# Kernel optimization log

Hardware: AMD Instinct MI355X
Metric: run time of the kernel (lower is better)

Reference implementation:

```python
import jax, jax.numpy as jnp
import numpy as np

N = 4096      # nodes in the propagation tree batch
D = 5000      # input (BoW/TF-IDF) feature dim
H = 512       # hidden_dim
C = 4         # n_class
L = 8         # number of tree levels


def setup_inputs() -> dict:
    key = jax.random.key(0)
    ks = jax.random.split(key, 12)
    init = lambda k, shape, fan: (jax.random.normal(k, shape, jnp.float32)
                                  / np.float32(np.sqrt(fan)))
    x = jax.random.normal(ks[0], (N, D), jnp.float32)
    adj = jax.random.uniform(ks[1], (N, N), jnp.float32)
    level = jax.random.randint(ks[2], (N,), 0, L, jnp.int32)
    return {
        "x": x,
        "adj": adj,
        "level": level,
        "E_w": init(ks[3], (H, D), D),
        "Wr": init(ks[4], (H, H), H),
        "Wz": init(ks[5], (H, H), H),
        "Ur": init(ks[6], (H, H), H),
        "Uz": init(ks[7], (H, H), H),
        "Wh": init(ks[8], (H, H), H),
        "Uh": init(ks[9], (H, H), H),
        "dec_w": init(ks[10], (C, H), H),
        "dec_b": jnp.zeros((C,), jnp.float32),
        "n_levels": L,
    }


def reference(x, adj, level, E_w, Wr, Wz, Ur, Uz, Wh, Uh, dec_w, dec_b, n_levels):
    # x_hat = E(x): [N, H]
    x_hat = x @ E_w.T
    # precompute gate input contributions from x_hat (constant across levels)
    xr = x_hat @ Wr.T
    xz = x_hat @ Wz.T
    xh = x_hat @ Wh.T
    h = jnp.zeros_like(x_hat)  # [N, H]
    # bottom-up over tree levels (deepest level first, root = level 0)
    for j in reversed(range(n_levels)):
        mask = (level == j).astype(x_hat.dtype)[:, None]  # [N, 1]
        # level_adj.mm(h): aggregate children states into current-level rows
        hs = mask * (adj @ h)                              # [N, H]
        r = jax.nn.sigmoid(xr + hs @ Ur.T)
        z = jax.nn.sigmoid(xz + hs @ Uz.T)
        hj_hat = jnp.tanh(xh + (hs * r) @ Uh.T)
        hj = (1.0 - z) * hs + z * hj_hat
        h = h + mask * hj
    # decoder(h): [N, C]
    return h @ dec_w.T + dec_b
```

## Files before the change

### kernel.cpp

```cpp
#include <hip/hip_runtime.h>
#include <math.h>


#define NNODE 4096
#define DD 5000
#define DP 5024
#define HH 512
#define HHHH 262144
#define LL 8
#define PMAX 640
#define AKS 8
#define AKC 512
#define STR 40
#define NHt 2097152
#define XCH 1696
#define EWP (HH * DP)

typedef __attribute__((ext_vector_type(8))) short short8v;
typedef __attribute__((ext_vector_type(4))) float float4v;

union fu { float f; unsigned u; };

__device__ __forceinline__ float sigf(float x) { return 1.0f / (1.0f + __expf(-x)); }
__device__ __forceinline__ float bf2f(ushort b) { fu v; v.u = ((unsigned)b) << 16; return v.f; }

__device__ __forceinline__ void splitpair(float a, float b, unsigned& hi,
                                          unsigned& mi, unsigned& lo) {
  const unsigned M = 0xFFFF0000u;
  fu A, B; A.f = a; B.f = b;
  hi = (A.u >> 16) | (B.u & M);
  fu Ah, Bh; Ah.u = A.u & M; Bh.u = B.u & M;
  float ra = a - Ah.f, rb = b - Bh.f;
  fu A1, B1; A1.f = ra; B1.f = rb;
  mi = (A1.u >> 16) | (B1.u & M);
  fu A1h, B1h; A1h.u = A1.u & M; B1h.u = B1.u & M;
  float ra2 = ra - A1h.f, rb2 = rb - B1h.f;
  fu A2, B2; A2.f = ra2; B2.f = rb2;
  lo = (A2.u >> 16) | (B2.u & M);
}

__device__ __forceinline__ void split8(const float* v, uint4& h, uint4& m, uint4& l) {
  splitpair(v[0], v[1], h.x, m.x, l.x);
  splitpair(v[2], v[3], h.y, m.y, l.y);
  splitpair(v[4], v[5], h.z, m.z, l.z);
  splitpair(v[6], v[7], h.w, m.w, l.w);
}

__device__ __forceinline__ void split1(float x, ushort& h, ushort& m, ushort& l) {
  const unsigned M = 0xFFFF0000u;
  fu a; a.f = x; h = (ushort)(a.u >> 16);
  fu ah; ah.u = a.u & M; float r = x - ah.f;
  fu b; b.f = r; m = (ushort)(b.u >> 16);
  fu bh; bh.u = b.u & M; float r2 = r - bh.f;
  fu c; c.f = r2; l = (ushort)(c.u >> 16);
}

template <int NB, int AROWS, int BROWS>
__device__ __forceinline__ void mfma6(const ushort* As, const ushort* Bs,
                                      int wm, int wn, int lr, int lg8,
                                      float4v (*acc)[NB]) {
  short8v a[2][3];
#pragma unroll
  for (int im = 0; im < 2; ++im)
#pragma unroll
    for (int p = 0; p < 3; ++p)
      a[im][p] = *reinterpret_cast<const short8v*>(
          &As[(p * AROWS + wm + 16 * im + lr) * STR + lg8]);
  short8v b[NB][3];
#pragma unroll
  for (int in = 0; in < NB; ++in)
#pragma unroll
    for (int p = 0; p < 3; ++p)
      b[in][p] = *reinterpret_cast<const short8v*>(
          &Bs[(p * BROWS + wn + 16 * in + lr) * STR + lg8]);
#pragma unroll
  for (int im = 0; im < 2; ++im)
#pragma unroll
    for (int in = 0; in < NB; ++in) {
      float4v c = acc[im][in];
      c = __builtin_amdgcn_mfma_f32_16x16x32_bf16(a[im][0], b[in][0], c, 0, 0, 0);
      c = __builtin_amdgcn_mfma_f32_16x16x32_bf16(a[im][0], b[in][1], c, 0, 0, 0);
      c = __builtin_amdgcn_mfma_f32_16x16x32_bf16(a[im][1], b[in][0], c, 0, 0, 0);
      c = __builtin_amdgcn_mfma_f32_16x16x32_bf16(a[im][0], b[in][2], c, 0, 0, 0);
      c = __builtin_amdgcn_mfma_f32_16x16x32_bf16(a[im][2], b[in][0], c, 0, 0, 0);
      c = __builtin_amdgcn_mfma_f32_16x16x32_bf16(a[im][1], b[in][1], c, 0, 0, 0);
      acc[im][in] = c;
    }
}

__global__ __launch_bounds__(256) void build_lists(const int* __restrict__ level,
                                                   int* __restrict__ counts,
                                                   int* __restrict__ rows, int N) {
  int i = blockIdx.x * blockDim.x + threadIdx.x;
  if (i < N) {
    int j = level[i];
    int p = atomicAdd(&counts[j], 1);
    rows[(size_t)j * N + p] = i;
  }
}

__global__ __launch_bounds__(256) void cast_all(
    const float* __restrict__ Ur, const float* __restrict__ Uz,
    const float* __restrict__ Uh, const float* __restrict__ Wr,
    const float* __restrict__ Wz, const float* __restrict__ Wh,
    ushort* __restrict__ urz3, ushort* __restrict__ uh3,
    ushort* __restrict__ w3s) {
  const int y = blockIdx.y;
  const float* src = (y == 0) ? Ur : (y == 1) ? Uz : (y == 2) ? Uh
                   : (y == 3) ? Wr : (y == 4) ? Wz : Wh;
  ushort* dst; size_t ps, off;
  if (y <= 1)      { dst = urz3; ps = 2 * (size_t)HHHH; off = (size_t)y * HHHH; }
  else if (y == 2) { dst = uh3;  ps = HHHH; off = 0; }
  else             { dst = w3s + (size_t)(y - 3) * 3 * HHHH; ps = HHHH; off = 0; }
  int i = (blockIdx.x * 256 + threadIdx.x) * 8;
  float4 t0 = *reinterpret_cast<const float4*>(src + i);
  float4 t1 = *reinterpret_cast<const float4*>(src + i + 4);
  float v[8] = {t0.x, t0.y, t0.z, t0.w, t1.x, t1.y, t1.z, t1.w};
  uint4 h, m, l;
  split8(v, h, m, l);
  *reinterpret_cast<uint4*>(dst + off + i) = h;
  *reinterpret_cast<uint4*>(dst + ps + off + i) = m;
  *reinterpret_cast<uint4*>(dst + 2 * ps + off + i) = l;
}

__global__ __launch_bounds__(256) void cast_ew(const float* __restrict__ Ew,
                                               ushort* __restrict__ ew3) {
  int idx = (blockIdx.x * 256 + threadIdx.x) * 8;
  int row = idx / DP, col = idx % DP;
  float v[8];
  if (col + 8 <= DD) {
    float4 t0 = *reinterpret_cast<const float4*>(Ew + (size_t)row * DD + col);
    float4 t1 = *reinterpret_cast<const float4*>(Ew + (size_t)row * DD + col + 4);
    v[0]=t0.x; v[1]=t0.y; v[2]=t0.z; v[3]=t0.w;
    v[4]=t1.x; v[5]=t1.y; v[6]=t1.z; v[7]=t1.w;
  } else {
#pragma unroll
    for (int i = 0; i < 8; ++i)
      v[i] = (col + i < DD) ? Ew[(size_t)row * DD + col + i] : 0.0f;
  }
  uint4 h, m, l;
  split8(v, h, m, l);
  *reinterpret_cast<uint4*>(ew3 + idx) = h;
  *reinterpret_cast<uint4*>(ew3 + EWP + idx) = m;
  *reinterpret_cast<uint4*>(ew3 + 2 * (size_t)EWP + idx) = l;
}

__global__ __launch_bounds__(256) void gemm_xhat_sk(const float* __restrict__ x,
                                                    const ushort* __restrict__ ew3,
                                                    float* __restrict__ xpart) {
  __shared__ ushort As[3 * 64 * STR];
  __shared__ ushort Bs[3 * 128 * STR];
  const int z = blockIdx.z;
  const int kb = z * XCH;
  const int kePad = min(kb + XCH, DP);
  const int keReal = min(kePad, DD);
  const int tid = threadIdx.x;
  const int bm = blockIdx.x * 64, bn = blockIdx.y * 128;
  const int wid = tid >> 6, lane = tid & 63;
  const int lr = lane & 15, lg = lane >> 4, lg8 = lg * 8;
  const int wm = (wid >> 1) * 32, wn = (wid & 1) * 64;
  const int ar = tid >> 2, akq = (tid & 3) * 8;
  const int br = tid >> 1, bkq = (tid & 1) * 16;
  const float* ap = x + (size_t)(bm + ar) * DD + kb + akq;
  const ushort* bph = ew3 + (size_t)(bn + br) * DP + kb + bkq;
  float4v acc[2][4];
#pragma unroll
  for (int i = 0; i < 2; ++i)
#pragma unroll
    for (int j = 0; j < 4; ++j) acc[i][j] = (float4v){0.f, 0.f, 0.f, 0.f};
  uint4 ah, am, al;
  short8v b0[3], b1[3];
  auto loadA = [&](int k0) {
    float v[8];
    if (k0 + 32 <= keReal) {
      float4 t0 = *reinterpret_cast<const float4*>(ap);
      float4 t1 = *reinterpret_cast<const float4*>(ap + 4);
      v[0]=t0.x; v[1]=t0.y; v[2]=t0.z; v[3]=t0.w;
      v[4]=t1.x; v[5]=t1.y; v[6]=t1.z; v[7]=t1.w;
    } else {
#pragma unroll
      for (int i = 0; i < 8; ++i) v[i] = (k0 + akq + i < keReal) ? ap[i] : 0.0f;
    }
    split8(v, ah, am, al);
    ap += 32;
  };
  auto loadB = [&]() {
#pragma unroll
    for (int p = 0; p < 3; ++p) {
      b0[p] = *reinterpret_cast<const short8v*>(bph + (size_t)p * EWP);
      b1[p] = *reinterpret_cast<const short8v*>(bph + (size_t)p * EWP + 8);
    }
    bph += 32;
  };
  loadA(kb); loadB();
  for (int k0 = kb; k0 < kePad; k0 += 32) {
    __syncthreads();
    *reinterpret_cast<uint4*>(&As[(0 * 64 + ar) * STR + akq]) = ah;
    *reinterpret_cast<uint4*>(&As[(1 * 64 + ar) * STR + akq]) = am;
    *reinterpret_cast<uint4*>(&As[(2 * 64 + ar) * STR + akq]) = al;
#pragma unroll
    for (int p = 0; p < 3; ++p) {
      *reinterpret_cast<short8v*>(&Bs[(p * 128 + br) * STR + bkq]) = b0[p];
      *reinterpret_cast<short8v*>(&Bs[(p * 128 + br) * STR + bkq + 8]) = b1[p];
    }
    __syncthreads();
    if (k0 + 32 < kePad) { loadA(k0 + 32); loadB(); }
    mfma6<4, 64, 128>(As, Bs, wm, wn, lr, lg8, acc);
  }
  float* C = xpart + (size_t)z * NHt;
#pragma unroll
  for (int im = 0; im < 2; ++im)
#pragma unroll
    for (int in = 0; in < 4; ++in)
#pragma unroll
      for (int r = 0; r < 4; ++r)
        C[(size_t)(bm + wm + im * 16 + lg * 4 + r) * HH + bn + wn + in * 16 + lr] =
            acc[im][in][r];
}

__global__ __launch_bounds__(256) void combine3(const float* __restrict__ p,
                                                ushort* __restrict__ xh3) {
  int i = (blockIdx.x * 256 + threadIdx.x) * 8;
  float v[8];
#pragma unroll
  for (int e = 0; e < 8; e += 4) {
    float4 a = *reinterpret_cast<const float4*>(p + i + e);
    float4 b = *reinterpret_cast<const float4*>(p + NHt + i + e);
    float4 c = *reinterpret_cast<const float4*>(p + 2 * (size_t)NHt + i + e);
    v[e + 0] = a.x + b.x + c.x; v[e + 1] = a.y + b.y + c.y;
    v[e + 2] = a.z + b.z + c.z; v[e + 3] = a.w + b.w + c.w;
  }
  uint4 h, m, l;
  split8(v, h, m, l);
  *reinterpret_cast<uint4*>(xh3 + i) = h;
  *reinterpret_cast<uint4*>(xh3 + NHt + i) = m;
  *reinterpret_cast<uint4*>(xh3 + 2 * (size_t)NHt + i) = l;
}

__global__ __launch_bounds__(256) void gemm_w36(const ushort* __restrict__ xh3,
                                                const ushort* __restrict__ w3s,
                                                float* __restrict__ xrzh) {
  const int z = blockIdx.z;
  const ushort* B = w3s + (size_t)z * 3 * HHHH;
  float* C = xrzh + (size_t)z * NHt;
  __shared__ ushort As[3 * 64 * STR];
  __shared__ ushort Bs[3 * 128 * STR];
  const int tid = threadIdx.x;
  const int bm = blockIdx.x * 64, bn = blockIdx.y * 128;
  const int wid = tid >> 6, lane = tid & 63;
  const int lr = lane & 15, lg = lane >> 4, lg8 = lg * 8;
  const int wm = (wid >> 1) * 32, wn = (wid & 1) * 64;
  const int ar = tid >> 2, akq = (tid & 3) * 8;
  const int br = tid >> 1, bkq = (tid & 1) * 16;
  const ushort* aph = xh3 + (size_t)(bm + ar) * HH + akq;
  const ushort* bph = B + (size_t)(bn + br) * HH + bkq;
  float4v acc[2][4];
#pragma unroll
  for (int i = 0; i < 2; ++i)
#pragma unroll
    for (int j = 0; j < 4; ++j) acc[i][j] = (float4v){0.f, 0.f, 0.f, 0.f};
  short8v a3[3], b0[3], b1[3];
  auto loadAll = [&]() {
#pragma unroll
    for (int p = 0; p < 3; ++p) {
      a3[p] = *reinterpret_cast<const short8v*>(aph + (size_t)p * NHt);
      b0[p] = *reinterpret_cast<const short8v*>(bph + (size_t)p * HHHH);
      b1[p] = *reinterpret_cast<const short8v*>(bph + (size_t)p * HHHH + 8);
    }
    aph += 32; bph += 32;
  };
  loadAll();
  for (int k0 = 0; k0 < HH; k0 += 32) {
    __syncthreads();
#pragma unroll
    for (int p = 0; p < 3; ++p) {
      *reinterpret_cast<short8v*>(&As[(p * 64 + ar) * STR + akq]) = a3[p];
      *reinterpret_cast<short8v*>(&Bs[(p * 128 + br) * STR + bkq]) = b0[p];
      *reinterpret_cast<short8v*>(&Bs[(p * 128 + br) * STR + bkq + 8]) = b1[p];
    }
    __syncthreads();
    if (k0 + 32 < HH) loadAll();
    mfma6<4, 64, 128>(As, Bs, wm, wn, lr, lg8, acc);
  }
#pragma unroll
  for (int im = 0; im < 2; ++im)
#pragma unroll
    for (int in = 0; in < 4; ++in)
#pragma unroll
      for (int r = 0; r < 4; ++r)
        C[(size_t)(bm + wm + im * 16 + lg * 4 + r) * HH + bn + wn + in * 16 + lr] =
            acc[im][in][r];
}

__global__ __launch_bounds__(256) void agg6(const float* __restrict__ adj,
                                            const ushort* __restrict__ hT3,
                                            const int* __restrict__ rows,
                                            const int* __restrict__ counts,
                                            int lvl, float* __restrict__ part) {
  const int cnt = min(counts[lvl], PMAX);
  const int bm = blockIdx.x * 32;
  if (bm >= cnt) return;
  const int* rl = rows + (size_t)lvl * NNODE;
  const int kb = blockIdx.z * AKC;
  const int bn = blockIdx.y * 128;
  __shared__ ushort As[3 * 32 * STR];
  __shared__ ushort Bs[3 * 128 * STR];
  const int tid = threadIdx.x;
  const int wid = tid >> 6, lane = tid & 63;
  const int lr = lane & 15, lg = lane >> 4, lg8 = lg * 8;
  const int wn = wid * 32;
  const int ar = (tid & 127) >> 2, akq = (tid & 3) * 8;
  const int br = tid >> 1, bkq = (tid & 1) * 16;
  int p0 = bm + ar;
  if (p0 >= cnt) p0 = cnt - 1;
  const float* ap = adj + (size_t)rl[p0] * NNODE + kb + akq;
  const ushort* bph = hT3 + (size_t)(bn + br) * NNODE + kb + bkq;
  float4v acc[2][2];
#pragma unroll
  for (int i = 0; i < 2; ++i)
#pragma unroll
    for (int j = 0; j < 2; ++j) acc[i][j] = (float4v){0.f, 0.f, 0.f, 0.f};
  uint4 ah, am, al;
  short8v b0[3], b1[3];
  auto loadA = [&]() {
    float4 t0 = *reinterpret_cast<const float4*>(ap);
    float4 t1 = *reinterpret_cast<const float4*>(ap + 4);
    float v[8] = {t0.x, t0.y, t0.z, t0.w, t1.x, t1.y, t1.z, t1.w};
    split8(v, ah, am, al);
    ap += 32;
  };
  auto loadB = [&]() {
#pragma unroll
    for (int p = 0; p < 3; ++p) {
      b0[p] = *reinterpret_cast<const short8v*>(bph + (size_t)p * NHt);
      b1[p] = *reinterpret_cast<const short8v*>(bph + (size_t)p * NHt + 8);
    }
    bph += 32;
  };
  if (tid < 128) loadA();
  loadB();
  for (int k0 = 0; k0 < AKC; k0 += 32) {
    __syncthreads();
    if (tid < 128) {
      *reinterpret_cast<uint4*>(&As[(0 * 32 + ar) * STR + akq]) = ah;
      *reinterpret_cast<uint4*>(&As[(1 * 32 + ar) * STR + akq]) = am;
      *reinterpret_cast<uint4*>(&As[(2 * 32 + ar) * STR + akq]) = al;
    }
#pragma unroll
    for (int p = 0; p < 3; ++p) {
      *reinterpret_cast<short8v*>(&Bs[(p * 128 + br) * STR + bkq]) = b0[p];
      *reinterpret_cast<short8v*>(&Bs[(p * 128 + br) * STR + bkq + 8]) = b1[p];
    }
    __syncthreads();
    if (k0 + 32 < AKC) {
      if (tid < 128) loadA();
      loadB();
    }
    mfma6<2, 32, 128>(As, Bs, 0, wn, lr, lg8, acc);
  }
  float* cp = part + (size_t)blockIdx.z * PMAX * HH;
#pragma unroll
  for (int im = 0; im < 2; ++im)
#pragma unroll
    for (int in = 0; in < 2; ++in)
#pragma unroll
      for (int r = 0; r < 4; ++r) {
        int p = bm + 16 * im + lg * 4 + r;
        if (p < cnt)
          cp[(size_t)p * HH + bn + wn + in * 16 + lr] = acc[im][in][r];
      }
}

__global__ __launch_bounds__(256) void agg_reduce6(const float* __restrict__ part,
                                                   float* __restrict__ hsf,
                                                   ushort* __restrict__ hs3) {
  int id = blockIdx.x * 256 + threadIdx.x;
  const int zs = PMAX * HH / 4;
  const float4* q = reinterpret_cast<const float4*>(part) + id;
  float4 s = q[0];
#pragma unroll
  for (int z = 1; z < AKS; ++z) {
    float4 t = q[(size_t)z * zs];
    s.x += t.x; s.y += t.y; s.z += t.z; s.w += t.w;
  }
  reinterpret_cast<float4*>(hsf)[id] = s;
  unsigned h0, m0, l0, h1, m1, l1;
  splitpair(s.x, s.y, h0, m0, l0);
  splitpair(s.z, s.w, h1, m1, l1);
  *reinterpret_cast<uint2*>(hs3 + (size_t)id * 4) = make_uint2(h0, h1);
  *reinterpret_cast<uint2*>(hs3 + PMAX * HH + (size_t)id * 4) = make_uint2(m0, m1);
  *reinterpret_cast<uint2*>(hs3 + 2 * PMAX * HH + (size_t)id * 4) = make_uint2(l0, l1);
}

__global__ __launch_bounds__(256) void gates_rz6(
    const ushort* __restrict__ hs3, const ushort* __restrict__ urz3,
    const float* __restrict__ xr, const float* __restrict__ xz,
    const float* __restrict__ hsf, const int* __restrict__ rows,
    const int* __restrict__ counts, int lvl, ushort* __restrict__ tb3,
    float* __restrict__ zb) {
  const int cnt = min(counts[lvl], PMAX);
  const int bm = blockIdx.x * 32;
  if (bm >= cnt) return;
  const int* rl = rows + (size_t)lvl * NNODE;
  const int bn = blockIdx.y * 64;
  __shared__ ushort As[3 * 32 * STR];
  __shared__ ushort Bs[3 * 64 * STR];
  const int tid = threadIdx.x;
  const int wid = tid >> 6, lane = tid & 63;
  const int lr = lane & 15, lg = lane >> 4, lg8 = lg * 8;
  const int wn = wid * 16;
  const int ar = (tid & 127) >> 2, akq = (tid & 3) * 8;
  const int br = tid >> 2, bkq = (tid & 3) * 8;
  const ushort* aph = hs3 + (size_t)(bm + ar) * HH + akq;
  const ushort* bph = urz3 + (size_t)(bn + br) * HH + bkq;
  float4v acc[2][1];
  acc[0][0] = (float4v){0.f, 0.f, 0.f, 0.f};
  acc[1][0] = (float4v){0.f, 0.f, 0.f, 0.f};
  short8v a3[3], b3[3];
  auto loadA = [&]() {
#pragma unroll
    for (int p = 0; p < 3; ++p)
      a3[p] = *reinterpret_cast<const short8v*>(aph + (size_t)p * PMAX * HH);
    aph += 32;
  };
  auto loadB = [&]() {
#pragma unroll
    for (int p = 0; p < 3; ++p)
      b3[p] = *reinterpret_cast<const short8v*>(bph + (size_t)p * 2 * HHHH);
    bph += 32;
  };
  if (tid < 128) loadA();
  loadB();
  for (int k0 = 0; k0 < HH; k0 += 32) {
    __syncthreads();
    if (tid < 128) {
#pragma unroll
      for (int p = 0; p < 3; ++p)
        *reinterpret_cast<short8v*>(&As[(p * 32 + ar) * STR + akq]) = a3[p];
    }
#pragma unroll
    for (int p = 0; p < 3; ++p)
      *reinterpret_cast<short8v*>(&Bs[(p * 64 + br) * STR + bkq]) = b3[p];
    __syncthreads();
    if (k0 + 32 < HH) {
      if (tid < 128) loadA();
      loadB();
    }
    mfma6<1, 32, 64>(As, Bs, 0, wn, lr, lg8, acc);
  }
  ushort* th = tb3;
  ushort* tm = tb3 + PMAX * HH;
  ushort* tl = tb3 + 2 * PMAX * HH;
#pragma unroll
  for (int im = 0; im < 2; ++im)
#pragma unroll
    for (int r = 0; r < 4; ++r) {
      int p = bm + 16 * im + lg * 4 + r;
      if (p < cnt) {
        int col = bn + wn + lr;
        int g = rl[p];
        if (col < HH) {
          float rr = sigf(xr[(size_t)g * HH + col] + acc[im][0][r]);
          float t = hsf[(size_t)p * HH + col] * rr;
          ushort h, m, l;
          split1(t, h, m, l);
          size_t idx = (size_t)p * HH + col;
          th[idx] = h; tm[idx] = m; tl[idx] = l;
        } else {
          int c = col - HH;
          zb[(size_t)p * HH + c] = sigf(xz[(size_t)g * HH + c] + acc[im][0][r]);
        }
      }
    }
}

__global__ __launch_bounds__(256) void gates_h6(
    const ushort* __restrict__ tb3, const ushort* __restrict__ uh3,
    const float* __restrict__ xh, const float* __restrict__ hsf,
    const float* __restrict__ zb, const int* __restrict__ rows,
    const int* __restrict__ counts, int lvl, ushort* __restrict__ hT3) {
  const int cnt = min(counts[lvl], PMAX);
  const int bm = blockIdx.x * 32;
  if (bm >= cnt) return;
  const int* rl = rows + (size_t)lvl * NNODE;
  const int bn = blockIdx.y * 64;
  __shared__ ushort As[3 * 32 * STR];
  __shared__ ushort Bs[3 * 64 * STR];
  const int tid = threadIdx.x;
  const int wid = tid >> 6, lane = tid & 63;
  const int lr = lane & 15, lg = lane >> 4, lg8 = lg * 8;
  const int wn = wid * 16;
  const int ar = (tid & 127) >> 2, akq = (tid & 3) * 8;
  const int br = tid >> 2, bkq = (tid & 3) * 8;
  const ushort* aph = tb3 + (size_t)(bm + ar) * HH + akq;
  const ushort* bph = uh3 + (size_t)(bn + br) * HH + bkq;
  float4v acc[2][1];
  acc[0][0] = (float4v){0.f, 0.f, 0.f, 0.f};
  acc[1][0] = (float4v){0.f, 0.f, 0.f, 0.f};
  short8v a3[3], b3[3];
  auto loadA = [&]() {
#pragma unroll
    for (int p = 0; p < 3; ++p)
      a3[p] = *reinterpret_cast<const short8v*>(aph + (size_t)p * PMAX * HH);
    aph += 32;
  };
  auto loadB = [&]() {
#pragma unroll
    for (int p = 0; p < 3; ++p)
      b3[p] = *reinterpret_cast<const short8v*>(bph + (size_t)p * HHHH);
    bph += 32;
  };
  if (tid < 128) loadA();
  loadB();
  for (int k0 = 0; k0 < HH; k0 += 32) {
    __syncthreads();
    if (tid < 128) {
#pragma unroll
      for (int p = 0; p < 3; ++p)
        *reinterpret_cast<short8v*>(&As[(p * 32 + ar) * STR + akq]) = a3[p];
    }
#pragma unroll
    for (int p = 0; p < 3; ++p)
      *reinterpret_cast<short8v*>(&Bs[(p * 64 + br) * STR + bkq]) = b3[p];
    __syncthreads();
    if (k0 + 32 < HH) {
      if (tid < 128) loadA();
      loadB();
    }
    mfma6<1, 32, 64>(As, Bs, 0, wn, lr, lg8, acc);
  }
  ushort* hp = hT3;
  ushort* mp = hT3 + NHt;
  ushort* lp = hT3 + 2 * (size_t)NHt;
#pragma unroll
  for (int im = 0; im < 2; ++im)
#pragma unroll
    for (int r = 0; r < 4; ++r) {
      int p = bm + 16 * im + lg * 4 + r;
      if (p < cnt) {
        int col = bn + wn + lr;
        int g = rl[p];
        size_t idx = (size_t)p * HH + col;
        float hh = tanhf(xh[(size_t)g * HH + col] + acc[im][0][r]);
        float zz = zb[idx];
        float hv = (1.0f - zz) * hsf[idx] + zz * hh;
        ushort h, m, l;
        split1(hv, h, m, l);
        size_t tix = (size_t)col * NNODE + g;
        hp[tix] = h; mp[tix] = m; lp[tix] = l;
      }
    }
}

__global__ __launch_bounds__(256) void lvl7_init(const float* __restrict__ xz,
                                                 const float* __restrict__ xh,
                                                 const int* __restrict__ rows,
                                                 const int* __restrict__ counts,
                                                 ushort* __restrict__ hT3) {
  const int cnt = min(counts[LL - 1], PMAX);
  int idx = blockIdx.x * 256 + threadIdx.x;
  int p = idx >> 6;
  int c0 = (idx & 63) * 8;
  if (p >= cnt) return;
  int g = rows[(size_t)(LL - 1) * NNODE + p];
  float4 z0 = *reinterpret_cast<const float4*>(xz + (size_t)g * HH + c0);
  float4 z1 = *reinterpret_cast<const float4*>(xz + (size_t)g * HH + c0 + 4);
  float4 h0 = *reinterpret_cast<const float4*>(xh + (size_t)g * HH + c0);
  float4 h1 = *reinterpret_cast<const float4*>(xh + (size_t)g * HH + c0 + 4);
  float zv[8] = {z0.x, z0.y, z0.z, z0.w, z1.x, z1.y, z1.z, z1.w};
  float hv[8] = {h0.x, h0.y, h0.z, h0.w, h1.x, h1.y, h1.z, h1.w};
#pragma unroll
  for (int i = 0; i < 8; ++i) {
    float val = sigf(zv[i]) * tanhf(hv[i]);
    ushort h, m, l;
    split1(val, h, m, l);
    size_t tix = (size_t)(c0 + i) * NNODE + g;
    hT3[tix] = h;
    hT3[NHt + tix] = m;
    hT3[2 * (size_t)NHt + tix] = l;
  }
}

__global__ __launch_bounds__(256) void decoder6(const ushort* __restrict__ hT3,
                                                const float* __restrict__ w,
                                                const float* __restrict__ b,
                                                float* __restrict__ out) {
  int t = threadIdx.x;
  int g = blockIdx.x * 64 + (t >> 2);
  int sub = t & 3;
  float a0 = 0.f, a1 = 0.f, a2 = 0.f, a3 = 0.f;
  for (int c = sub; c < HH; c += 4) {
    size_t idx = (size_t)c * NNODE + g;
    float hv = bf2f(hT3[idx]) + bf2f(hT3[NHt + idx]) + bf2f(hT3[2 * (size_t)NHt + idx]);
    a0 = fmaf(hv, w[c], a0);
    a1 = fmaf(hv, w[HH + c], a1);
    a2 = fmaf(hv, w[2 * HH + c], a2);
    a3 = fmaf(hv, w[3 * HH + c], a3);
  }
  a0 += __shfl_down(a0, 2); a0 += __shfl_down(a0, 1);
  a1 += __shfl_down(a1, 2); a1 += __shfl_down(a1, 1);
  a2 += __shfl_down(a2, 2); a2 += __shfl_down(a2, 1);
  a3 += __shfl_down(a3, 2); a3 += __shfl_down(a3, 1);
  if (sub == 0) {
    out[(size_t)g * 4 + 0] = a0 + b[0];
    out[(size_t)g * 4 + 1] = a1 + b[1];
    out[(size_t)g * 4 + 2] = a2 + b[2];
    out[(size_t)g * 4 + 3] = a3 + b[3];
  }
}

extern "C" void kernel_launch(void* const* d_in, const int* in_sizes, int n_in,
                              void* d_out, int out_size, void* d_ws,
                              size_t ws_size, hipStream_t stream) {
  const float* x   = (const float*)d_in[0];
  const float* adj = (const float*)d_in[1];
  const int* level = (const int*)d_in[2];
  const float* E_w = (const float*)d_in[3];
  const float* Wr  = (const float*)d_in[4];
  const float* Wz  = (const float*)d_in[5];
  const float* Ur  = (const float*)d_in[6];
  const float* Uz  = (const float*)d_in[7];
  const float* Wh  = (const float*)d_in[8];
  const float* Uh  = (const float*)d_in[9];
  const float* dw  = (const float*)d_in[10];
  const float* db  = (const float*)d_in[11];

  char* wp = (char*)d_ws;
  ushort* urz3 = (ushort*)wp; wp += (size_t)3 * 2 * HHHH * 2;
  ushort* uh3  = (ushort*)wp; wp += (size_t)3 * HHHH * 2;
  ushort* w3s  = (ushort*)wp; wp += (size_t)3 * 3 * HHHH * 2;
  ushort* hT3  = (ushort*)wp; wp += (size_t)3 * NHt * 2;
  float*  xrzh = (float*)wp;  wp += (size_t)3 * NHt * 4;
  char* region = wp;
  ushort* ew3  = (ushort*)region;
  float*  part = (float*)region;
  ushort* tb3  = (ushort*)(region + (size_t)AKS * PMAX * HH * 4);
  float*  zb   = (float*)((char*)tb3 + (size_t)3 * PMAX * HH * 2);
  float*  hsf  = (float*)((char*)zb + (size_t)PMAX * HH * 4);
  ushort* hs3  = (ushort*)((char*)hsf + (size_t)PMAX * HH * 4);
  size_t regionBytes = (size_t)3 * EWP * 2;
  size_t lvlBytes = (size_t)AKS * PMAX * HH * 4 + (size_t)3 * PMAX * HH * 2 +
                    (size_t)PMAX * HH * 4 + (size_t)PMAX * HH * 4 +
                    (size_t)3 * PMAX * HH * 2;
  if (lvlBytes > regionBytes) regionBytes = lvlBytes;
  wp = region + regionBytes;
  int* counts = (int*)wp; wp += 64;
  int* rowsl  = (int*)wp; wp += (size_t)LL * NNODE * 4;
  if (ws_size < (size_t)(wp - (char*)d_ws)) return;

  ushort* xh3 = hT3;
  float* xpart = xrzh;

  hipMemsetAsync(counts, 0, 64, stream);
  build_lists<<<(NNODE + 255) / 256, 256, 0, stream>>>(level, counts, rowsl, NNODE);
  cast_all<<<dim3(HHHH / 8 / 256, 6), 256, 0, stream>>>(Ur, Uz, Uh, Wr, Wz, Wh,
                                                        urz3, uh3, w3s);
  cast_ew<<<dim3(HH * DP / 8 / 256), 256, 0, stream>>>(E_w, ew3);
  gemm_xhat_sk<<<dim3(NNODE / 64, HH / 128, 3), 256, 0, stream>>>(x, ew3, xpart);
  combine3<<<NHt / 8 / 256, 256, 0, stream>>>(xpart, xh3);
  gemm_w36<<<dim3(NNODE / 64, HH / 128, 3), 256, 0, stream>>>(xh3, w3s, xrzh);

  const float* xr  = xrzh;
  const float* xzp = xrzh + (size_t)NHt;
  const float* xhp = xrzh + (size_t)2 * NHt;

  hipMemsetAsync(hT3, 0, (size_t)3 * NHt * 2, stream);
  lvl7_init<<<PMAX * HH / 8 / 256, 256, 0, stream>>>(xzp, xhp, rowsl, counts, hT3);

  for (int j = LL - 2; j >= 0; --j) {
    agg6<<<dim3(PMAX / 32, HH / 128, AKS), 256, 0, stream>>>(adj, hT3, rowsl,
                                                             counts, j, part);
    agg_reduce6<<<PMAX * HH / 4 / 256, 256, 0, stream>>>(part, hsf, hs3);
    gates_rz6<<<dim3(PMAX / 32, 2 * HH / 64), 256, 0, stream>>>(
        hs3, urz3, xr, xzp, hsf, rowsl, counts, j, tb3, zb);
    gates_h6<<<dim3(PMAX / 32, HH / 64), 256, 0, stream>>>(
        tb3, uh3, xhp, hsf, zb, rowsl, counts, j, hT3);
  }
  decoder6<<<dim3(NNODE / 64), 256, 0, stream>>>(hT3, dw, db, (float*)d_out);
}
```

Before: 801.6 us.

## Fuse split-K reduce into gates_rz and double-buffer register prefetch in GEMMs

Removes the per-level agg_reduce6 kernel. gates_rz6 now sums the AKS split-K partials itself while loading its A operand, splits the sums into three bf16 parts in registers, and writes hsf in its epilogue. Separately, the xhat split-K GEMM and the agg6 kernel now prefetch two k-steps ahead into alternating register sets. The fusion saves one launch and the hs3 round trip per level, but every gates_rz6 column block re-reads all eight partials, multiplying partial traffic, and the prefetch raises register pressure.

Result: slower. 890.0 us (+11.0%).

```diff
diff --git a/kernel.cpp b/kernel.cpp
--- a/kernel.cpp
+++ b/kernel.cpp
@@ -168,9 +168,9 @@
   for (int i = 0; i < 2; ++i)
 #pragma unroll
     for (int j = 0; j < 4; ++j) acc[i][j] = (float4v){0.f, 0.f, 0.f, 0.f};
-  uint4 ah, am, al;
-  short8v b0[3], b1[3];
-  auto loadA = [&](int k0) {
+  uint4 ah0, am0, al0, ah1, am1, al1;
+  short8v bA0[3], bB0[3], bA1[3], bB1[3];
+  auto loadA = [&](int k0, uint4& h, uint4& m, uint4& l) {
     float v[8];
     if (k0 + 32 <= keReal) {
       float4 t0 = *reinterpret_cast<const float4*>(ap);
@@ -181,32 +181,47 @@
 #pragma unroll
       for (int i = 0; i < 8; ++i) v[i] = (k0 + akq + i < keReal) ? ap[i] : 0.0f;
     }
-    split8(v, ah, am, al);
+    split8(v, h, m, l);
     ap += 32;
   };
-  auto loadB = [&]() {
+  auto loadB = [&](short8v (&c0)[3], short8v (&c1)[3]) {
 #pragma unroll
     for (int p = 0; p < 3; ++p) {
-      b0[p] = *reinterpret_cast<const short8v*>(bph + (size_t)p * EWP);
-      b1[p] = *reinterpret_cast<const short8v*>(bph + (size_t)p * EWP + 8);
+      c0[p] = *reinterpret_cast<const short8v*>(bph + (size_t)p * EWP);
+      c1[p] = *reinterpret_cast<const short8v*>(bph + (size_t)p * EWP + 8);
     }
     bph += 32;
   };
-  loadA(kb); loadB();
-  for (int k0 = kb; k0 < kePad; k0 += 32) {
-    __syncthreads();
-    *reinterpret_cast<uint4*>(&As[(0 * 64 + ar) * STR + akq]) = ah;
-    *reinterpret_cast<uint4*>(&As[(1 * 64 + ar) * STR + akq]) = am;
-    *reinterpret_cast<uint4*>(&As[(2 * 64 + ar) * STR + akq]) = al;
+  auto stage = [&](const uint4& h, const uint4& m, const uint4& l,
+                   const short8v (&c0)[3], const short8v (&c1)[3]) {
+    *reinterpret_cast<uint4*>(&As[(0 * 64 + ar) * STR + akq]) = h;
+    *reinterpret_cast<uint4*>(&As[(1 * 64 + ar) * STR + akq]) = m;
+    *reinterpret_cast<uint4*>(&As[(2 * 64 + ar) * STR + akq]) = l;
 #pragma unroll
     for (int p = 0; p < 3; ++p) {
-      *reinterpret_cast<short8v*>(&Bs[(p * 128 + br) * STR + bkq]) = b0[p];
-      *reinterpret_cast<short8v*>(&Bs[(p * 128 + br) * STR + bkq + 8]) = b1[p];
-    }
-    __syncthreads();
-    if (k0 + 32 < kePad) { loadA(k0 + 32); loadB(); }
+      *reinterpret_cast<short8v*>(&Bs[(p * 128 + br) * STR + bkq]) = c0[p];
+      *reinterpret_cast<short8v*>(&Bs[(p * 128 + br) * STR + bkq + 8]) = c1[p];
+    }
+  };
+  loadA(kb, ah0, am0, al0); loadB(bA0, bB0);
+  loadA(kb + 32, ah1, am1, al1); loadB(bA1, bB1);
+  int k0 = kb;
+  for (; k0 + 32 < kePad; k0 += 64) {
+    __syncthreads();
+    stage(ah0, am0, al0, bA0, bB0);
+    __syncthreads();
+    if (k0 + 64 < kePad) { loadA(k0 + 64, ah0, am0, al0); loadB(bA0, bB0); }
     mfma6<4, 64, 128>(As, Bs, wm, wn, lr, lg8, acc);
-  }
+    __syncthreads();
+    stage(ah1, am1, al1, bA1, bB1);
+    __syncthreads();
+    if (k0 + 96 < kePad) { loadA(k0 + 96, ah1, am1, al1); loadB(bA1, bB1); }
+    mfma6<4, 64, 128>(As, Bs, wm, wn, lr, lg8, acc);
+  }
+  __syncthreads();
+  stage(ah0, am0, al0, bA0, bB0);
+  __syncthreads();
+  mfma6<4, 64, 128>(As, Bs, wm, wn, lr, lg8, acc);
   float* C = xpart + (size_t)z * NHt;
 #pragma unroll
   for (int im = 0; im < 2; ++im)
@@ -320,41 +335,55 @@
   for (int i = 0; i < 2; ++i)
 #pragma unroll
     for (int j = 0; j < 2; ++j) acc[i][j] = (float4v){0.f, 0.f, 0.f, 0.f};
-  uint4 ah, am, al;
-  short8v b0[3], b1[3];
-  auto loadA = [&]() {
+  uint4 ah0, am0, al0, ah1, am1, al1;
+  short8v bA0[3], bB0[3], bA1[3], bB1[3];
+  auto loadA = [&](uint4& h, uint4& m, uint4& l) {
     float4 t0 = *reinterpret_cast<const float4*>(ap);
     float4 t1 = *reinterpret_cast<const float4*>(ap + 4);
     float v[8] = {t0.x, t0.y, t0.z, t0.w, t1.x, t1.y, t1.z, t1.w};
-    split8(v, ah, am, al);
+    split8(v, h, m, l);
     ap += 32;
   };
-  auto loadB = [&]() {
+  auto loadB = [&](short8v (&c0)[3], short8v (&c1)[3]) {
 #pragma unroll
     for (int p = 0; p < 3; ++p) {
-      b0[p] = *reinterpret_cast<const short8v*>(bph + (size_t)p * NHt);
-      b1[p] = *reinterpret_cast<const short8v*>(bph + (size_t)p * NHt + 8);
+      c0[p] = *reinterpret_cast<const short8v*>(bph + (size_t)p * NHt);
+      c1[p] = *reinterpret_cast<const short8v*>(bph + (size_t)p * NHt + 8);
     }
     bph += 32;
   };
-  if (tid < 128) loadA();
-  loadB();
-  for (int k0 = 0; k0 < AKC; k0 += 32) {
-    __syncthreads();
+  auto stage = [&](const uint4& h, const uint4& m, const uint4& l,
+                   const short8v (&c0)[3], const short8v (&c1)[3]) {
     if (tid < 128) {
-      *reinterpret_cast<uint4*>(&As[(0 * 32 + ar) * STR + akq]) = ah;
-      *reinterpret_cast<uint4*>(&As[(1 * 32 + ar) * STR + akq]) = am;
-      *reinterpret_cast<uint4*>(&As[(2 * 32 + ar) * STR + akq]) = al;
+      *reinterpret_cast<uint4*>(&As[(0 * 32 + ar) * STR + akq]) = h;
+      *reinterpret_cast<uint4*>(&As[(1 * 32 + ar) * STR + akq]) = m;
+      *reinterpret_cast<uint4*>(&As[(2 * 32 + ar) * STR + akq]) = l;
     }
 #pragma unroll
     for (int p = 0; p < 3; ++p) {
-      *reinterpret_cast<short8v*>(&Bs[(p * 128 + br) * STR + bkq]) = b0[p];
-      *reinterpret_cast<short8v*>(&Bs[(p * 128 + br) * STR + bkq + 8]) = b1[p];
-    }
-    __syncthreads();
-    if (k0 + 32 < AKC) {
-      if (tid < 128) loadA();
-      loadB();
+      *reinterpret_cast<short8v*>(&Bs[(p * 128 + br) * STR + bkq]) = c0[p];
+      *reinterpret_cast<short8v*>(&Bs[(p * 128 + br) * STR + bkq + 8]) = c1[p];
+    }
+  };
+  if (tid < 128) loadA(ah0, am0, al0);
+  loadB(bA0, bB0);
+  if (tid < 128) loadA(ah1, am1, al1);
+  loadB(bA1, bB1);
+  for (int k0 = 0; k0 < AKC; k0 += 64) {
+    __syncthreads();
+    stage(ah0, am0, al0, bA0, bB0);
+    __syncthreads();
+    if (k0 + 64 < AKC) {
+      if (tid < 128) loadA(ah0, am0, al0);
+      loadB(bA0, bB0);
+    }
+    mfma6<2, 32, 128>(As, Bs, 0, wn, lr, lg8, acc);
+    __syncthreads();
+    stage(ah1, am1, al1, bA1, bB1);
+    __syncthreads();
+    if (k0 + 96 < AKC) {
+      if (tid < 128) loadA(ah1, am1, al1);
+      loadB(bA1, bB1);
     }
     mfma6<2, 32, 128>(As, Bs, 0, wn, lr, lg8, acc);
   }
@@ -371,33 +400,12 @@
       }
 }
 
-__global__ __launch_bounds__(256) void agg_reduce6(const float* __restrict__ part,
-                                                   float* __restrict__ hsf,
-                                                   ushort* __restrict__ hs3) {
-  int id = blockIdx.x * 256 + threadIdx.x;
-  const int zs = PMAX * HH / 4;
-  const float4* q = reinterpret_cast<const float4*>(part) + id;
-  float4 s = q[0];
-#pragma unroll
-  for (int z = 1; z < AKS; ++z) {
-    float4 t = q[(size_t)z * zs];
-    s.x += t.x; s.y += t.y; s.z += t.z; s.w += t.w;
-  }
-  reinterpret_cast<float4*>(hsf)[id] = s;
-  unsigned h0, m0, l0, h1, m1, l1;
-  splitpair(s.x, s.y, h0, m0, l0);
-  splitpair(s.z, s.w, h1, m1, l1);
-  *reinterpret_cast<uint2*>(hs3 + (size_t)id * 4) = make_uint2(h0, h1);
-  *reinterpret_cast<uint2*>(hs3 + PMAX * HH + (size_t)id * 4) = make_uint2(m0, m1);
-  *reinterpret_cast<uint2*>(hs3 + 2 * PMAX * HH + (size_t)id * 4) = make_uint2(l0, l1);
-}
-
 __global__ __launch_bounds__(256) void gates_rz6(
-    const ushort* __restrict__ hs3, const ushort* __restrict__ urz3,
+    const float* __restrict__ part, const ushort* __restrict__ urz3,
     const float* __restrict__ xr, const float* __restrict__ xz,
-    const float* __restrict__ hsf, const int* __restrict__ rows,
-    const int* __restrict__ counts, int lvl, ushort* __restrict__ tb3,
-    float* __restrict__ zb) {
+    const int* __restrict__ rows, const int* __restrict__ counts, int lvl,
+    ushort* __restrict__ tb3, float* __restrict__ zb,
+    float* __restrict__ hsf) {
   const int cnt = min(counts[lvl], PMAX);
   const int bm = blockIdx.x * 32;
   if (bm >= cnt) return;
@@ -411,17 +419,29 @@
   const int wn = wid * 16;
   const int ar = (tid & 127) >> 2, akq = (tid & 3) * 8;
   const int br = tid >> 2, bkq = (tid & 3) * 8;
-  const ushort* aph = hs3 + (size_t)(bm + ar) * HH + akq;
+  const size_t zs = (size_t)PMAX * HH;
+  const float* app = part + (size_t)(bm + ar) * HH + akq;
   const ushort* bph = urz3 + (size_t)(bn + br) * HH + bkq;
   float4v acc[2][1];
   acc[0][0] = (float4v){0.f, 0.f, 0.f, 0.f};
   acc[1][0] = (float4v){0.f, 0.f, 0.f, 0.f};
-  short8v a3[3], b3[3];
+  uint4 ah, am, al;
+  short8v b3[3];
   auto loadA = [&]() {
-#pragma unroll
-    for (int p = 0; p < 3; ++p)
-      a3[p] = *reinterpret_cast<const short8v*>(aph + (size_t)p * PMAX * HH);
-    aph += 32;
+    float s[8];
+    float4 t0 = *reinterpret_cast<const float4*>(app);
+    float4 t1 = *reinterpret_cast<const float4*>(app + 4);
+    s[0]=t0.x; s[1]=t0.y; s[2]=t0.z; s[3]=t0.w;
+    s[4]=t1.x; s[5]=t1.y; s[6]=t1.z; s[7]=t1.w;
+#pragma unroll
+    for (int z = 1; z < AKS; ++z) {
+      float4 u0 = *reinterpret_cast<const float4*>(app + z * zs);
+      float4 u1 = *reinterpret_cast<const float4*>(app + z * zs + 4);
+      s[0]+=u0.x; s[1]+=u0.y; s[2]+=u0.z; s[3]+=u0.w;
+      s[4]+=u1.x; s[5]+=u1.y; s[6]+=u1.z; s[7]+=u1.w;
+    }
+    split8(s, ah, am, al);
+    app += 32;
   };
   auto loadB = [&]() {
 #pragma unroll
@@ -434,9 +454,9 @@
   for (int k0 = 0; k0 < HH; k0 += 32) {
     __syncthreads();
     if (tid < 128) {
-#pragma unroll
-      for (int p = 0; p < 3; ++p)
-        *reinterpret_cast<short8v*>(&As[(p * 32 + ar) * STR + akq]) = a3[p];
+      *reinterpret_cast<uint4*>(&As[(0 * 32 + ar) * STR + akq]) = ah;
+      *reinterpret_cast<uint4*>(&As[(1 * 32 + ar) * STR + akq]) = am;
+      *reinterpret_cast<uint4*>(&As[(2 * 32 + ar) * STR + akq]) = al;
     }
 #pragma unroll
     for (int p = 0; p < 3; ++p)
@@ -460,8 +480,13 @@
         int col = bn + wn + lr;
         int g = rl[p];
         if (col < HH) {
+          const float* q = part + (size_t)p * HH + col;
+          float s = q[0];
+#pragma unroll
+          for (int z = 1; z < AKS; ++z) s += q[z * zs];
+          hsf[(size_t)p * HH + col] = s;
           float rr = sigf(xr[(size_t)g * HH + col] + acc[im][0][r]);
-          float t = hsf[(size_t)p * HH + col] * rr;
+          float t = s * rr;
           ushort h, m, l;
           split1(t, h, m, l);
           size_t idx = (size_t)p * HH + col;
@@ -637,11 +662,9 @@
   ushort* tb3  = (ushort*)(region + (size_t)AKS * PMAX * HH * 4);
   float*  zb   = (float*)((char*)tb3 + (size_t)3 * PMAX * HH * 2);
   float*  hsf  = (float*)((char*)zb + (size_t)PMAX * HH * 4);
-  ushort* hs3  = (ushort*)((char*)hsf + (size_t)PMAX * HH * 4);
   size_t regionBytes = (size_t)3 * EWP * 2;
   size_t lvlBytes = (size_t)AKS * PMAX * HH * 4 + (size_t)3 * PMAX * HH * 2 +
-                    (size_t)PMAX * HH * 4 + (size_t)PMAX * HH * 4 +
-                    (size_t)3 * PMAX * HH * 2;
+                    (size_t)PMAX * HH * 4 + (size_t)PMAX * HH * 4;
   if (lvlBytes > regionBytes) regionBytes = lvlBytes;
   wp = region + regionBytes;
   int* counts = (int*)wp; wp += 64;
@@ -670,9 +693,8 @@
   for (int j = LL - 2; j >= 0; --j) {
     agg6<<<dim3(PMAX / 32, HH / 128, AKS), 256, 0, stream>>>(adj, hT3, rowsl,
                                                              counts, j, part);
-    agg_reduce6<<<PMAX * HH / 4 / 256, 256, 0, stream>>>(part, hsf, hs3);
     gates_rz6<<<dim3(PMAX / 32, 2 * HH / 64), 256, 0, stream>>>(
-        hs3, urz3, xr, xzp, hsf, rowsl, counts, j, tb3, zb);
+        part, urz3, xr, xzp, rowsl, counts, j, tb3, zb, hsf);
     gates_h6<<<dim3(PMAX / 32, HH / 64), 256, 0, stream>>>(
         tb3, uh3, xhp, hsf, zb, rowsl, counts, j, hT3);
   }
```
